# Performance work log

Measured on AMD Instinct MI355X. Metric: run time of the kernel, lower is better.

Reference implementation:

```python
import jax, jax.numpy as jnp
import numpy as np

B, T, D = 32, 512, 768
DUR_MAX = 8.0


def length_regulate(x, dur):
    # dur[dur < 0] = 0; reps = (dur + 0.5).long()  (floor of dur+0.5 for dur >= 0)
    dur = jnp.maximum(dur, 0.0)
    reps = jnp.floor(dur + 0.5).astype(jnp.int32)          # [B, T]
    cum = jnp.cumsum(reps, axis=1)                          # [B, T] end offsets
    totals = cum[:, -1]                                     # [B] per-sample lengths
    t_out = int(jnp.max(totals))                            # padded output length (data-dependent, eager)
    pos = jnp.arange(t_out, dtype=jnp.int32)                # [Tout]
    # For output slot j, source token index = searchsorted(cum, j, 'right')
    idx = jax.vmap(lambda c: jnp.searchsorted(c, pos, side='right'))(cum)  # [B, Tout]
    idx = jnp.minimum(idx, x.shape[1] - 1)                  # clamp padding region
    out = jnp.take_along_axis(x, idx[..., None], axis=1)    # [B, Tout, D] gather
    mask = pos[None, :] < totals[:, None]                   # [B, Tout]
    return jnp.where(mask[..., None], out, jnp.zeros((), x.dtype))


def setup_inputs() -> dict:
    key = jax.random.key(0)
    k1, k2 = jax.random.split(key)
    x = jax.random.normal(k1, (B, T, D), dtype=jnp.float32)
    dur = jax.random.uniform(k2, (B, T), dtype=jnp.float32, minval=0.0, maxval=DUR_MAX)
    return {"x": x, "dur": dur}


def reference(x, dur):
    return length_regulate(x, dur)
```

## Files before the change

### kernel.cpp

```cpp
#include <hip/hip_runtime.h>

#define BB 32
#define TT 512
#define DD 768
#define VEC_PER_ROW (DD / 4)
#define TOK_PER_BLOCK 8
#define BLOCKS_PER_BATCH (TT / TOK_PER_BLOCK)

typedef float f4 __attribute__((ext_vector_type(4)));

__global__ __launch_bounds__(TT) void lr_scan_kernel(
    const float* __restrict__ dur, int* __restrict__ cum) {
    __shared__ int s[TT];
    const int b = blockIdx.x;
    const int t = threadIdx.x;
    float d = dur[b * TT + t];
    d = fmaxf(d, 0.0f);
    s[t] = (int)floorf(d + 0.5f);
    __syncthreads();
    #pragma unroll
    for (int off = 1; off < TT; off <<= 1) {
        int v = (t >= off) ? s[t - off] : 0;
        __syncthreads();
        s[t] += v;
        __syncthreads();
    }
    cum[b * TT + t] = s[t];
}

__global__ __launch_bounds__(VEC_PER_ROW) void lr_scatter_kernel(
    const float* __restrict__ x, const int* __restrict__ cum,
    float* __restrict__ out, int t_out) {
    __shared__ int scum[TT];
    const int b = blockIdx.y;
    const int tid = threadIdx.x;

    for (int i = tid; i < TT; i += VEC_PER_ROW) scum[i] = cum[b * TT + i];
    __syncthreads();

    const int s0 = blockIdx.x * TOK_PER_BLOCK;
    const f4* xb = (const f4*)(x + (size_t)b * TT * DD);
    f4* ob = (f4*)(out + (size_t)b * (size_t)t_out * DD);

    #pragma unroll
    for (int k = 0; k < TOK_PER_BLOCK; ++k) {
        const int t = s0 + k;
        const int start = (t == 0) ? 0 : scum[t - 1];
        const int end = scum[t];
        if (end > start) {
            const f4 v = xb[(size_t)t * VEC_PER_ROW + tid];
            for (int p = start; p < end; ++p)
                __builtin_nontemporal_store(v, &ob[(size_t)p * VEC_PER_ROW + tid]);
        }
    }

    const int total = scum[TT - 1];
    const f4 z = (f4)(0.0f);
    for (int pos = total + blockIdx.x; pos < t_out; pos += BLOCKS_PER_BATCH)
        __builtin_nontemporal_store(z, &ob[(size_t)pos * VEC_PER_ROW + tid]);
}

extern "C" void kernel_launch(void* const* d_in, const int* in_sizes, int n_in,
                              void* d_out, int out_size, void* d_ws, size_t ws_size,
                              hipStream_t stream) {
    const float* x   = (const float*)d_in[0];
    const float* dur = (const float*)d_in[1];
    float* out = (float*)d_out;
    int* cum = (int*)d_ws;

    const int t_out = out_size / (BB * DD);

    lr_scan_kernel<<<BB, TT, 0, stream>>>(dur, cum);

    dim3 sgrid(BLOCKS_PER_BATCH, BB);
    lr_scatter_kernel<<<sgrid, VEC_PER_ROW, 0, stream>>>(x, cum, out, t_out);
}
```

Baseline: 255.7 us.

## Fuse duration scan into scatter kernel, recomputing prefix sum per block

Removes the separate scan kernel and workspace round-trip. Each scatter block now loads the durations itself and computes the prefix sum in shared memory with a 192-thread Hillis-Steele scan covering three elements per thread. This saves a kernel launch and the dependency between the two kernels. In exchange, the scan is repeated redundantly in all 64 blocks per batch row, adding about 18 barrier-separated steps before any copying starts.

```diff
diff --git a/kernel.cpp b/kernel.cpp
--- a/kernel.cpp
+++ b/kernel.cpp
@@ -3,40 +3,37 @@
 #define BB 32
 #define TT 512
 #define DD 768
-#define VEC_PER_ROW (DD / 4)
+#define NTHREADS 192
 #define TOK_PER_BLOCK 8
 #define BLOCKS_PER_BATCH (TT / TOK_PER_BLOCK)
 
 typedef float f4 __attribute__((ext_vector_type(4)));
 
-__global__ __launch_bounds__(TT) void lr_scan_kernel(
-    const float* __restrict__ dur, int* __restrict__ cum) {
-    __shared__ int s[TT];
-    const int b = blockIdx.x;
-    const int t = threadIdx.x;
-    float d = dur[b * TT + t];
-    d = fmaxf(d, 0.0f);
-    s[t] = (int)floorf(d + 0.5f);
-    __syncthreads();
-    #pragma unroll
-    for (int off = 1; off < TT; off <<= 1) {
-        int v = (t >= off) ? s[t - off] : 0;
-        __syncthreads();
-        s[t] += v;
-        __syncthreads();
-    }
-    cum[b * TT + t] = s[t];
-}
-
-__global__ __launch_bounds__(VEC_PER_ROW) void lr_scatter_kernel(
-    const float* __restrict__ x, const int* __restrict__ cum,
+__global__ __launch_bounds__(NTHREADS) void lr_fused_kernel(
+    const float* __restrict__ x, const float* __restrict__ dur,
     float* __restrict__ out, int t_out) {
     __shared__ int scum[TT];
     const int b = blockIdx.y;
     const int tid = threadIdx.x;
 
-    for (int i = tid; i < TT; i += VEC_PER_ROW) scum[i] = cum[b * TT + i];
+    for (int i = tid; i < TT; i += NTHREADS) {
+        float d = fmaxf(dur[b * TT + i], 0.0f);
+        scum[i] = (int)floorf(d + 0.5f);
+    }
     __syncthreads();
+
+    #pragma unroll
+    for (int off = 1; off < TT; off <<= 1) {
+        const int i0 = tid, i1 = tid + NTHREADS, i2 = tid + 2 * NTHREADS;
+        int v0 = (i0 >= off) ? scum[i0 - off] : 0;
+        int v1 = (i1 >= off) ? scum[i1 - off] : 0;
+        int v2 = (i2 < TT && i2 >= off) ? scum[i2 - off] : 0;
+        __syncthreads();
+        scum[i0] += v0;
+        scum[i1] += v1;
+        if (i2 < TT) scum[i2] += v2;
+        __syncthreads();
+    }
 
     const int s0 = blockIdx.x * TOK_PER_BLOCK;
     const f4* xb = (const f4*)(x + (size_t)b * TT * DD);
@@ -48,16 +45,16 @@
         const int start = (t == 0) ? 0 : scum[t - 1];
         const int end = scum[t];
         if (end > start) {
-            const f4 v = xb[(size_t)t * VEC_PER_ROW + tid];
+            const f4 v = xb[(size_t)t * NTHREADS + tid];
             for (int p = start; p < end; ++p)
-                __builtin_nontemporal_store(v, &ob[(size_t)p * VEC_PER_ROW + tid]);
+                __builtin_nontemporal_store(v, &ob[(size_t)p * NTHREADS + tid]);
         }
     }
 
     const int total = scum[TT - 1];
     const f4 z = (f4)(0.0f);
     for (int pos = total + blockIdx.x; pos < t_out; pos += BLOCKS_PER_BATCH)
-        __builtin_nontemporal_store(z, &ob[(size_t)pos * VEC_PER_ROW + tid]);
+        __builtin_nontemporal_store(z, &ob[(size_t)pos * NTHREADS + tid]);
 }
 
 extern "C" void kernel_launch(void* const* d_in, const int* in_sizes, int n_in,
@@ -66,12 +63,10 @@
     const float* x   = (const float*)d_in[0];
     const float* dur = (const float*)d_in[1];
     float* out = (float*)d_out;
-    int* cum = (int*)d_ws;
+    (void)d_ws; (void)ws_size;
 
     const int t_out = out_size / (BB * DD);
 
-    lr_scan_kernel<<<BB, TT, 0, stream>>>(dur, cum);
-
-    dim3 sgrid(BLOCKS_PER_BATCH, BB);
-    lr_scatter_kernel<<<sgrid, VEC_PER_ROW, 0, stream>>>(x, cum, out, t_out);
+    dim3 grid(BLOCKS_PER_BATCH, BB);
+    lr_fused_kernel<<<grid, NTHREADS, 0, stream>>>(x, dur, out, t_out);
 }
```

New measurement: 254.1 us. No clear change (-0.6%).
